# Kernel tuning notes

Measured on AMD Instinct MI355X. Metric: run time of the kernel, lower is better.

Reference implementation:

```python
import jax, jax.numpy as jnp
import numpy as np

B = 4096          # batch
D = 512           # nOut (embedding dim)
N_CLASSES = 5994  # nClasses (VoxCeleb2 speakers)


def setup_inputs() -> dict:
    key = jax.random.key(0)
    k = jax.random.split(key, 6)
    return {
        "x": jax.random.normal(k[0], (B, D), dtype=jnp.float32),
        "label": jax.random.randint(k[1], (B,), 0, N_CLASSES),
        "centers": jax.random.normal(k[2], (N_CLASSES, D), dtype=jnp.float32),
        "fc_w": jax.random.normal(k[3], (1, D), dtype=jnp.float32) / np.sqrt(D),
        "fc_b": jnp.zeros((1,), dtype=jnp.float32),
        "ch_w": jax.random.normal(k[4], (N_CLASSES, D), dtype=jnp.float32) / np.sqrt(D),
        "ch_b": jnp.zeros((N_CLASSES,), dtype=jnp.float32),
    }


def _ce(logits, labels):
    # mean cross-entropy, single stable log-softmax
    logp = jax.nn.log_softmax(logits, axis=-1)
    return -jnp.mean(jnp.take_along_axis(logp, labels[:, None], axis=-1))


def _center_add(x, label, n_classes):
    """Faithful sequential label-wise running average from the torch loop:
    first occurrence of label l: cadd[l] += x[i]; later: cadd[l] = (cadd[l]+x[i])/2.
    Sequential recurrence -> lax.scan over the batch."""
    d = x.shape[1]

    def step(carry, inp):
        cadd, seen = carry
        xi, li = inp
        first = seen[li] == 0
        row = cadd[li]
        new_row = jnp.where(first, row + xi, 0.5 * (row + xi))
        return (cadd.at[li].set(new_row), seen.at[li].set(1)), None

    init = (jnp.zeros((n_classes, d), x.dtype), jnp.zeros((n_classes,), jnp.int32))
    (cadd, seen), _ = jax.lax.scan(step, init, (x, label))
    return cadd, seen.astype(x.dtype)


def reference(x, label, centers, fc_w, fc_b, ch_w, ch_b):
    n_classes = centers.shape[0]
    cadd, label_add = _center_add(x, label, n_classes)  # label_add == labels present in batch

    alpha = jax.nn.sigmoid(centers @ fc_w.T + fc_b)[:, 0]        # [nClasses]
    center_mask = 1.0 - label_add
    gate = alpha * label_add + center_mask                        # [nClasses]
    new_center = centers * gate[:, None] + cadd * ((1.0 - alpha) * label_add)[:, None]

    center_logits = new_center @ ch_w.T + ch_b                    # [nClasses, nClasses]
    lossC = _ce(center_logits, jnp.arange(n_classes))

    output = x @ ch_w.T + ch_b                                    # [B, nClasses]
    nloss = _ce(output, label)

    prec1 = 100.0 * jnp.mean((jnp.argmax(output, axis=-1) == label).astype(jnp.float32))
    return nloss + lossC, prec1
```

## Files before the change

kernel.cpp:

```cpp
#include <hip/hip_runtime.h>

#define BB 4096
#define DD 512
#define NCC 5994
#define RBX 64
#define RBC 94
#define NSL 12
#define TPS 4
#define NBLK ((RBX + RBC) * NSL)
#define PSZ (NSL * (BB + NCC))

typedef __attribute__((ext_vector_type(8))) short bfx8;
typedef __attribute__((ext_vector_type(8))) unsigned short usx8;
typedef __attribute__((ext_vector_type(4))) float fx4;

__device__ __forceinline__ unsigned short f2bf(float f) {
    unsigned u = __builtin_bit_cast(unsigned, f);
    u += 0x7fff + ((u >> 16) & 1);
    return (unsigned short)(u >> 16);
}

__device__ __forceinline__ void gload_lds16(const void* g, void* l) {
    __builtin_amdgcn_global_load_lds(
        (const __attribute__((address_space(1))) void*)g,
        (__attribute__((address_space(3))) void*)l, 16, 0, 0);
}

__global__ void prep_kernel(const int* __restrict__ label, float* __restrict__ w,
                            float* __restrict__ label_add, const float* __restrict__ x,
                            unsigned short* __restrict__ xbuf, float* __restrict__ cadd) {
    __shared__ int lab[BB];
    int b = blockIdx.x, t = threadIdx.x;
    if (b < 16) {
        for (int j = t; j < BB; j += 256) lab[j] = label[j];
        __syncthreads();
        int i = b * 256 + t;
        int li = lab[i];
        int cnt = 0, rank = 0;
        for (int j = 0; j < BB; ++j) {
            int e = (lab[j] == li) ? 1 : 0;
            cnt += e;
            if (j < i) rank += e;
        }
        float expo = (rank == 0) ? (float)(cnt - 1) : (float)(cnt - rank);
        w[i] = exp2f(-expo);
        label_add[li] = 1.0f;
    } else if (b < 784) {
        int base = (b - 16) * 256 + t;
        float4 z = make_float4(0.f, 0.f, 0.f, 0.f);
        float4* c4 = (float4*)cadd;
#pragma unroll
        for (int k = 0; k < 4; ++k) {
            int idx = base + k * 196608;
            if (idx < (NCC * DD) / 4) c4[idx] = z;
        }
    } else {
        int i = (b - 784) * 256 + t;
        const float4* g = (const float4*)(x + (size_t)i * 8);
        float4 v0 = g[0], v1 = g[1];
        usx8 u;
        u[0] = f2bf(v0.x); u[1] = f2bf(v0.y); u[2] = f2bf(v0.z); u[3] = f2bf(v0.w);
        u[4] = f2bf(v1.x); u[5] = f2bf(v1.y); u[6] = f2bf(v1.z); u[7] = f2bf(v1.w);
        *(usx8*)(xbuf + (size_t)i * 8) = u;
    }
}

__global__ void cadd_kernel(const float* __restrict__ x, const int* __restrict__ label,
                            const float* __restrict__ w, float* __restrict__ cadd) {
    int i = blockIdx.x;
    int li = label[i];
    float wi = w[i];
    const float* xr = x + (size_t)i * DD;
    float* cr = cadd + (size_t)li * DD;
    int t = threadIdx.x;
    atomicAdd(&cr[t], wi * xr[t]);
    atomicAdd(&cr[t + 256], wi * xr[t + 256]);
}

__global__ void newcenter_kernel(const float* __restrict__ centers,
                                 const float* __restrict__ fc_w,
                                 const float* __restrict__ fc_b,
                                 const float* __restrict__ cadd,
                                 const float* __restrict__ label_add,
                                 unsigned short* __restrict__ ncb) {
    int l = blockIdx.x;
    int t = threadIdx.x;
    const float* cr = centers + (size_t)l * DD;
    float part = fmaf(cr[t], fc_w[t], cr[t + 256] * fc_w[t + 256]);
#pragma unroll
    for (int off = 32; off; off >>= 1) part += __shfl_xor(part, off);
    __shared__ float wsum[4];
    if ((t & 63) == 0) wsum[t >> 6] = part;
    __syncthreads();
    float dot = wsum[0] + wsum[1] + wsum[2] + wsum[3] + fc_b[0];
    float alpha = 1.0f / (1.0f + expf(-dot));
    float la = label_add[l];
    float gate = alpha * la + (1.0f - la);
    float beta = (1.0f - alpha) * la;
    const float* car = cadd + (size_t)l * DD;
    unsigned short* nr = ncb + (size_t)l * DD;
    nr[t]       = f2bf(fmaf(cr[t],       gate, car[t]       * beta));
    nr[t + 256] = f2bf(fmaf(cr[t + 256], gate, car[t + 256] * beta));
}

__global__ void convw_kernel(const float* __restrict__ src, unsigned short* __restrict__ dst) {
    int i = blockIdx.x * 256 + threadIdx.x;
    if (i >= NCC * DD / 8) return;
    const float4* g = (const float4*)(src + (size_t)i * 8);
    float4 v0 = g[0], v1 = g[1];
    usx8 u;
    u[0] = f2bf(v0.x); u[1] = f2bf(v0.y); u[2] = f2bf(v0.z); u[3] = f2bf(v0.w);
    u[4] = f2bf(v1.x); u[5] = f2bf(v1.y); u[6] = f2bf(v1.z); u[7] = f2bf(v1.w);
    *(usx8*)(dst + (size_t)i * 8) = u;
}

__global__ __launch_bounds__(256, 3) void mfma_ce_kernel(
    const unsigned short* __restrict__ xb, const unsigned short* __restrict__ ncb,
    const unsigned short* __restrict__ wb, const float* __restrict__ chb,
    const int* __restrict__ labelg,
    float* __restrict__ pm, float* __restrict__ ps, float* __restrict__ pt,
    float* __restrict__ pv, int* __restrict__ pi)
{
    __shared__ short lA[2][64 * 64];
    __shared__ short lB[2][128 * 64];

    int b = blockIdx.x;
    int xm, rb, slice, nrows;
    const unsigned short* src;
    if (b < RBX * NSL) { xm = 1; rb = b % RBX; slice = b / RBX; nrows = BB;  src = xb; }
    else { int c = b - RBX * NSL; xm = 0; rb = c % RBC; slice = c / RBC; nrows = NCC; src = ncb; }
    int row0  = rb * 64;
    int tile0 = slice * TPS;

    int t = threadIdx.x, lane = t & 63, wv = t >> 6;
    int wm = wv >> 1, wn = wv & 1;
    int l15 = lane & 15, l4 = lane >> 4;

    int sk8 = (lane & 7) ^ ((lane >> 3) & 7);
    int r0q = min(row0 + wv * 16 + (lane >> 3), nrows - 1);
    int r1q = min(row0 + wv * 16 + 8 + (lane >> 3), nrows - 1);
    const unsigned short* aQ0 = src + (size_t)r0q * DD + sk8 * 8;
    const unsigned short* aQ1 = src + (size_t)r1q * DD + sk8 * 8;
    int colq = wv * 32 + (lane >> 3);

    int l4x   = l4 ^ (l15 & 3);
    int ksx   = (l15 >> 2) & 1;
    int slot0 = ((0 ^ ksx) << 2) | l4x;
    int slot1 = ((1 ^ ksx) << 2) | l4x;
    int aoff0 = (wm * 32 + l15) * 128 + slot0 * 16;
    int aoff1 = (wm * 32 + l15) * 128 + slot1 * 16;
    int boff0 = (wn * 64 + l15) * 128 + slot0 * 16;
    int boff1 = (wn * 64 + l15) * 128 + slot1 * 16;

    float m_[2][4], s_[2][4], tg_[2][4], av_[2][4];
    int ai_[2][4], tc_[2][4];
#pragma unroll
    for (int mf = 0; mf < 2; ++mf)
#pragma unroll
        for (int j = 0; j < 4; ++j) {
            m_[mf][j] = -1e30f; s_[mf][j] = 0.f; tg_[mf][j] = 0.f;
            av_[mf][j] = -1e30f; ai_[mf][j] = 0x7fffffff;
            int grow = row0 + wm * 32 + mf * 16 + l4 * 4 + j;
            tc_[mf][j] = xm ? labelg[min(grow, BB - 1)] : grow;
        }

    auto stage = [&](int s, int bufIdx) {
        int tile = tile0 + (s >> 3);
        int ko = (s & 7) * 64;
        gload_lds16(aQ0 + ko, &lA[bufIdx][wv * 1024]);
        gload_lds16(aQ1 + ko, &lA[bufIdx][wv * 1024 + 512]);
        int cb = tile * 128 + colq;
#pragma unroll
        for (int q = 0; q < 4; ++q) {
            const unsigned short* bs =
                wb + (size_t)min(cb + q * 8, NCC - 1) * DD + sk8 * 8 + ko;
            gload_lds16(bs, &lB[bufIdx][wv * 2048 + q * 512]);
        }
    };

    stage(0, 0);
    __syncthreads();

    fx4 acc[2][4];
    float biasv[4];
    int buf = 0;

    for (int s = 0; s < TPS * 8; ++s) {
        int kc = s & 7;
        int tile = tile0 + (s >> 3);
        if (s + 1 < TPS * 8) stage(s + 1, buf ^ 1);
        if (kc == 0) {
#pragma unroll
            for (int mf = 0; mf < 2; ++mf)
#pragma unroll
                for (int nf = 0; nf < 4; ++nf) {
                    fx4 z = {0.f, 0.f, 0.f, 0.f};
                    acc[mf][nf] = z;
                }
#pragma unroll
            for (int nf = 0; nf < 4; ++nf) {
                int col = tile * 128 + wn * 64 + nf * 16 + l15;
                biasv[nf] = (col < NCC) ? chb[col] : 0.f;
            }
        }
        const char* Ab = (const char*)lA[buf];
        const char* Bb = (const char*)lB[buf];
        {
            bfx8 a0 = *(const bfx8*)(Ab + aoff0);
            bfx8 a1 = *(const bfx8*)(Ab + aoff0 + 2048);
            bfx8 b0 = *(const bfx8*)(Bb + boff0);
            bfx8 b1 = *(const bfx8*)(Bb + boff0 + 2048);
            bfx8 b2 = *(const bfx8*)(Bb + boff0 + 4096);
            bfx8 b3 = *(const bfx8*)(Bb + boff0 + 6144);
            acc[0][0] = __builtin_amdgcn_mfma_f32_16x16x32_bf16(a0, b0, acc[0][0], 0, 0, 0);
            acc[0][1] = __builtin_amdgcn_mfma_f32_16x16x32_bf16(a0, b1, acc[0][1], 0, 0, 0);
            acc[0][2] = __builtin_amdgcn_mfma_f32_16x16x32_bf16(a0, b2, acc[0][2], 0, 0, 0);
            acc[0][3] = __builtin_amdgcn_mfma_f32_16x16x32_bf16(a0, b3, acc[0][3], 0, 0, 0);
            acc[1][0] = __builtin_amdgcn_mfma_f32_16x16x32_bf16(a1, b0, acc[1][0], 0, 0, 0);
            acc[1][1] = __builtin_amdgcn_mfma_f32_16x16x32_bf16(a1, b1, acc[1][1], 0, 0, 0);
            acc[1][2] = __builtin_amdgcn_mfma_f32_16x16x32_bf16(a1, b2, acc[1][2], 0, 0, 0);
            acc[1][3] = __builtin_amdgcn_mfma_f32_16x16x32_bf16(a1, b3, acc[1][3], 0, 0, 0);
        }
        {
            bfx8 a0 = *(const bfx8*)(Ab + aoff1);
            bfx8 a1 = *(const bfx8*)(Ab + aoff1 + 2048);
            bfx8 b0 = *(const bfx8*)(Bb + boff1);
            bfx8 b1 = *(const bfx8*)(Bb + boff1 + 2048);
            bfx8 b2 = *(const bfx8*)(Bb + boff1 + 4096);
            bfx8 b3 = *(const bfx8*)(Bb + boff1 + 6144);
            acc[0][0] = __builtin_amdgcn_mfma_f32_16x16x32_bf16(a0, b0, acc[0][0], 0, 0, 0);
            acc[0][1] = __builtin_amdgcn_mfma_f32_16x16x32_bf16(a0, b1, acc[0][1], 0, 0, 0);
            acc[0][2] = __builtin_amdgcn_mfma_f32_16x16x32_bf16(a0, b2, acc[0][2], 0, 0, 0);
            acc[0][3] = __builtin_amdgcn_mfma_f32_16x16x32_bf16(a0, b3, acc[0][3], 0, 0, 0);
            acc[1][0] = __builtin_amdgcn_mfma_f32_16x16x32_bf16(a1, b0, acc[1][0], 0, 0, 0);
            acc[1][1] = __builtin_amdgcn_mfma_f32_16x16x32_bf16(a1, b1, acc[1][1], 0, 0, 0);
            acc[1][2] = __builtin_amdgcn_mfma_f32_16x16x32_bf16(a1, b2, acc[1][2], 0, 0, 0);
            acc[1][3] = __builtin_amdgcn_mfma_f32_16x16x32_bf16(a1, b3, acc[1][3], 0, 0, 0);
        }

        if (kc == 7) {
            int colb = tile * 128 + wn * 64 + l15;
#pragma unroll
            for (int mf = 0; mf < 2; ++mf)
#pragma unroll
                for (int j = 0; j < 4; ++j) {
                    float v0 = (colb      < NCC) ? acc[mf][0][j] + biasv[0] : -1e30f;
                    float v1 = (colb + 16 < NCC) ? acc[mf][1][j] + biasv[1] : -1e30f;
                    float v2 = (colb + 32 < NCC) ? acc[mf][2][j] + biasv[2] : -1e30f;
                    float v3 = (colb + 48 < NCC) ? acc[mf][3][j] + biasv[3] : -1e30f;
                    float cmax = fmaxf(fmaxf(v0, v1), fmaxf(v2, v3));
                    float nm = fmaxf(m_[mf][j], cmax);
                    float sacc = s_[mf][j] * __expf(m_[mf][j] - nm);
                    if (colb      < NCC) sacc += __expf(v0 - nm);
                    if (colb + 16 < NCC) sacc += __expf(v1 - nm);
                    if (colb + 32 < NCC) sacc += __expf(v2 - nm);
                    if (colb + 48 < NCC) sacc += __expf(v3 - nm);
                    s_[mf][j] = sacc;
                    m_[mf][j] = nm;
                    if (xm) {
                        if (v0 > av_[mf][j]) { av_[mf][j] = v0; ai_[mf][j] = colb; }
                        if (v1 > av_[mf][j]) { av_[mf][j] = v1; ai_[mf][j] = colb + 16; }
                        if (v2 > av_[mf][j]) { av_[mf][j] = v2; ai_[mf][j] = colb + 32; }
                        if (v3 > av_[mf][j]) { av_[mf][j] = v3; ai_[mf][j] = colb + 48; }
                    }
                    int d = tc_[mf][j] - colb;
                    if (d == 0)  tg_[mf][j] = v0;
                    if (d == 16) tg_[mf][j] = v1;
                    if (d == 32) tg_[mf][j] = v2;
                    if (d == 48) tg_[mf][j] = v3;
                }
        }
        __syncthreads();
        buf ^= 1;
    }

#pragma unroll
    for (int off = 1; off < 16; off <<= 1) {
#pragma unroll
        for (int mf = 0; mf < 2; ++mf)
#pragma unroll
            for (int j = 0; j < 4; ++j) {
                float om = __shfl_xor(m_[mf][j], off);
                float os = __shfl_xor(s_[mf][j], off);
                float ot = __shfl_xor(tg_[mf][j], off);
                float ov = __shfl_xor(av_[mf][j], off);
                int   oi = __shfl_xor(ai_[mf][j], off);
                float nm = fmaxf(m_[mf][j], om);
                s_[mf][j] = s_[mf][j] * __expf(m_[mf][j] - nm) + os * __expf(om - nm);
                m_[mf][j] = nm;
                tg_[mf][j] += ot;
                if (ov > av_[mf][j] || (ov == av_[mf][j] && oi < ai_[mf][j])) {
                    av_[mf][j] = ov; ai_[mf][j] = oi;
                }
            }
    }

    float* red = (float*)lB;
    int* redi = (int*)(red + 512);
    if (l15 == 0) {
#pragma unroll
        for (int mf = 0; mf < 2; ++mf)
#pragma unroll
            for (int j = 0; j < 4; ++j) {
                int rowloc = wm * 32 + mf * 16 + l4 * 4 + j;
                int idx = wn * 64 + rowloc;
                red[idx]       = m_[mf][j];
                red[128 + idx] = s_[mf][j];
                red[256 + idx] = tg_[mf][j];
                red[384 + idx] = av_[mf][j];
                redi[idx]      = ai_[mf][j];
            }
    }
    __syncthreads();
    if (t < 64) {
        int grow = row0 + t;
        if (grow < nrows) {
            float M = red[t], S = red[128 + t], T = red[256 + t];
            float V = red[384 + t]; int I = redi[t];
            float m2 = red[64 + t], s2 = red[192 + t];
            float nm = fmaxf(M, m2);
            S = S * __expf(M - nm) + s2 * __expf(m2 - nm); M = nm;
            T += red[320 + t];
            float v2 = red[448 + t]; int i2 = redi[64 + t];
            if (v2 > V || (v2 == V && i2 < I)) { V = v2; I = i2; }
            int pidx = xm ? (grow * NSL + slice) : (BB * NSL + grow * NSL + slice);
            pm[pidx] = M; ps[pidx] = S; pt[pidx] = T; pv[pidx] = V; pi[pidx] = I;
        }
    }
}

__global__ void merge_kernel(const float* __restrict__ pm, const float* __restrict__ ps,
                             const float* __restrict__ pt, const float* __restrict__ pv,
                             const int* __restrict__ pi, const int* __restrict__ label,
                             float* __restrict__ sums) {
    int tid = blockIdx.x * 256 + threadIdx.x;
    float ce = 0.f, corr = 0.f;
    int isx = (tid < BB) ? 1 : 0;
    int base = -1;
    if (tid < BB) base = tid * NSL;
    else if (tid < BB + NCC) base = BB * NSL + (tid - BB) * NSL;
    if (base >= 0) {
        float M = -1e30f, S = 0.f, T = 0.f, V = -1e30f; int I = 0x7fffffff;
#pragma unroll
        for (int s2 = 0; s2 < NSL; ++s2) {
            float m = pm[base + s2], s = ps[base + s2];
            float nm = fmaxf(M, m);
            S = S * __expf(M - nm) + s * __expf(m - nm); M = nm;
            T += pt[base + s2];
            float v = pv[base + s2]; int i2 = pi[base + s2];
            if (v > V || (v == V && i2 < I)) { V = v; I = i2; }
        }
        ce = -(T - M - logf(S));
        if (isx) corr = (I == label[tid]) ? 1.f : 0.f;
    }
#pragma unroll
    for (int off = 32; off; off >>= 1) {
        ce += __shfl_xor(ce, off);
        corr += __shfl_xor(corr, off);
    }
    if ((threadIdx.x & 63) == 0) {
        atomicAdd(&sums[isx ? 0 : 2], ce);
        if (isx) atomicAdd(&sums[1], corr);
    }
}

__global__ void finalize_kernel(const float* __restrict__ sums, float* __restrict__ out) {
    out[0] = sums[0] / (float)BB + sums[2] / (float)NCC;
    out[1] = 100.0f * sums[1] / (float)BB;
}

extern "C" void kernel_launch(void* const* d_in, const int* in_sizes, int n_in,
                              void* d_out, int out_size, void* d_ws, size_t ws_size,
                              hipStream_t stream) {
    const float* x       = (const float*)d_in[0];
    const int*   label   = (const int*)d_in[1];
    const float* centers = (const float*)d_in[2];
    const float* fc_w    = (const float*)d_in[3];
    const float* fc_b    = (const float*)d_in[4];
    const float* ch_w    = (const float*)d_in[5];
    const float* ch_b    = (const float*)d_in[6];
    float* out = (float*)d_out;

    float* ws = (float*)d_ws;
    float* w         = ws;
    float* label_add = ws + 4096;
    float* sums      = ws + 10090;
    float* cadd      = ws + 14192;
    float* pm        = ws + 14192;
    float* ps        = pm + PSZ;
    float* pt        = ps + PSZ;
    float* pv        = pt + PSZ;
    int*   pi        = (int*)(pv + PSZ);
    unsigned short* wbuf  = (unsigned short*)(ws + 619592);
    unsigned short* xbuf  = (unsigned short*)(ws + 3084144);
    unsigned short* ncbuf = (unsigned short*)(ws + 4132720);

    hipMemsetAsync(label_add, 0, 6000 * sizeof(float), stream);

    prep_kernel<<<1808, 256, 0, stream>>>(label, w, label_add, x, xbuf, cadd);
    cadd_kernel<<<BB, 256, 0, stream>>>(x, label, w, cadd);
    newcenter_kernel<<<NCC, 256, 0, stream>>>(centers, fc_w, fc_b, cadd, label_add, ncbuf);
    convw_kernel<<<(NCC * DD / 8 + 255) / 256, 256, 0, stream>>>(ch_w, wbuf);

    mfma_ce_kernel<<<NBLK, 256, 0, stream>>>(xbuf, ncbuf, wbuf, ch_b, label,
                                             pm, ps, pt, pv, pi);

    merge_kernel<<<(BB + NCC + 255) / 256, 256, 0, stream>>>(pm, ps, pt, pv, pi, label, sums);
    finalize_kernel<<<1, 1, 0, stream>>>(sums, out);
}
```

Baseline: 315.0 us.

## Restructure GEMM main loop with explicit waitcnt barriers, hoisted bias, merged argmax

Splits the K loop into an unrolled tile loop with an inner k-chunk loop, replaces __syncthreads with a partial vmcnt wait plus raw s_barrier so the next stage's global-to-LDS loads stay in flight, and raises wave priority around the MFMA block. Bias values for all four tiles are preloaded into registers up front. The separate argmax value tracker is dropped and the argmax index now rides on the running softmax max, which removes registers, shuffles and LDS traffic. It also issues a wasted wraparound stage on the last step, and correctness depends on the vmcnt count matching the six loads per stage.

New measurement: 366.5 us. +16.3%, slower.

```diff
diff --git a/kernel.cpp b/kernel.cpp
--- a/kernel.cpp
+++ b/kernel.cpp
@@ -152,14 +152,23 @@
     int boff0 = (wn * 64 + l15) * 128 + slot0 * 16;
     int boff1 = (wn * 64 + l15) * 128 + slot1 * 16;
 
-    float m_[2][4], s_[2][4], tg_[2][4], av_[2][4];
+    float bva[4][4];
+#pragma unroll
+    for (int tt = 0; tt < 4; ++tt)
+#pragma unroll
+        for (int nf = 0; nf < 4; ++nf) {
+            int col = (tile0 + tt) * 128 + wn * 64 + nf * 16 + l15;
+            bva[tt][nf] = (col < NCC) ? chb[col] : 0.f;
+        }
+
+    float m_[2][4], s_[2][4], tg_[2][4];
     int ai_[2][4], tc_[2][4];
 #pragma unroll
     for (int mf = 0; mf < 2; ++mf)
 #pragma unroll
         for (int j = 0; j < 4; ++j) {
             m_[mf][j] = -1e30f; s_[mf][j] = 0.f; tg_[mf][j] = 0.f;
-            av_[mf][j] = -1e30f; ai_[mf][j] = 0x7fffffff;
+            ai_[mf][j] = 0x7fffffff;
             int grow = row0 + wm * 32 + mf * 16 + l4 * 4 + j;
             tc_[mf][j] = xm ? labelg[min(grow, BB - 1)] : grow;
         }
@@ -179,39 +188,44 @@
     };
 
     stage(0, 0);
-    __syncthreads();
 
     fx4 acc[2][4];
-    float biasv[4];
     int buf = 0;
 
-    for (int s = 0; s < TPS * 8; ++s) {
-        int kc = s & 7;
-        int tile = tile0 + (s >> 3);
-        if (s + 1 < TPS * 8) stage(s + 1, buf ^ 1);
-        if (kc == 0) {
-#pragma unroll
-            for (int mf = 0; mf < 2; ++mf)
-#pragma unroll
-                for (int nf = 0; nf < 4; ++nf) {
-                    fx4 z = {0.f, 0.f, 0.f, 0.f};
-                    acc[mf][nf] = z;
-                }
+#pragma unroll
+    for (int tt = 0; tt < 4; ++tt) {
+#pragma unroll
+        for (int mf = 0; mf < 2; ++mf)
 #pragma unroll
             for (int nf = 0; nf < 4; ++nf) {
-                int col = tile * 128 + wn * 64 + nf * 16 + l15;
-                biasv[nf] = (col < NCC) ? chb[col] : 0.f;
+                fx4 z = {0.f, 0.f, 0.f, 0.f};
+                acc[mf][nf] = z;
             }
-        }
-        const char* Ab = (const char*)lA[buf];
-        const char* Bb = (const char*)lB[buf];
-        {
+
+        for (int s2 = 0; s2 < 8; ++s2) {
+            int step = tt * 8 + s2;
+            int nxt = (step + 1 < 32) ? step + 1 : 0;
+            stage(nxt, buf ^ 1);
+            asm volatile("s_waitcnt vmcnt(6)" ::: "memory");
+            __builtin_amdgcn_s_barrier();
+            __builtin_amdgcn_sched_barrier(0);
+
+            const char* Ab = (const char*)lA[buf];
+            const char* Bb = (const char*)lB[buf];
             bfx8 a0 = *(const bfx8*)(Ab + aoff0);
             bfx8 a1 = *(const bfx8*)(Ab + aoff0 + 2048);
             bfx8 b0 = *(const bfx8*)(Bb + boff0);
             bfx8 b1 = *(const bfx8*)(Bb + boff0 + 2048);
             bfx8 b2 = *(const bfx8*)(Bb + boff0 + 4096);
             bfx8 b3 = *(const bfx8*)(Bb + boff0 + 6144);
+            bfx8 a2 = *(const bfx8*)(Ab + aoff1);
+            bfx8 a3 = *(const bfx8*)(Ab + aoff1 + 2048);
+            bfx8 b4 = *(const bfx8*)(Bb + boff1);
+            bfx8 b5 = *(const bfx8*)(Bb + boff1 + 2048);
+            bfx8 b6 = *(const bfx8*)(Bb + boff1 + 4096);
+            bfx8 b7 = *(const bfx8*)(Bb + boff1 + 6144);
+
+            __builtin_amdgcn_s_setprio(1);
             acc[0][0] = __builtin_amdgcn_mfma_f32_16x16x32_bf16(a0, b0, acc[0][0], 0, 0, 0);
             acc[0][1] = __builtin_amdgcn_mfma_f32_16x16x32_bf16(a0, b1, acc[0][1], 0, 0, 0);
             acc[0][2] = __builtin_amdgcn_mfma_f32_16x16x32_bf16(a0, b2, acc[0][2], 0, 0, 0);
@@ -220,49 +234,43 @@
             acc[1][1] = __builtin_amdgcn_mfma_f32_16x16x32_bf16(a1, b1, acc[1][1], 0, 0, 0);
             acc[1][2] = __builtin_amdgcn_mfma_f32_16x16x32_bf16(a1, b2, acc[1][2], 0, 0, 0);
             acc[1][3] = __builtin_amdgcn_mfma_f32_16x16x32_bf16(a1, b3, acc[1][3], 0, 0, 0);
-        }
+            acc[0][0] = __builtin_amdgcn_mfma_f32_16x16x32_bf16(a2, b4, acc[0][0], 0, 0, 0);
+            acc[0][1] = __builtin_amdgcn_mfma_f32_16x16x32_bf16(a2, b5, acc[0][1], 0, 0, 0);
+            acc[0][2] = __builtin_amdgcn_mfma_f32_16x16x32_bf16(a2, b6, acc[0][2], 0, 0, 0);
+            acc[0][3] = __builtin_amdgcn_mfma_f32_16x16x32_bf16(a2, b7, acc[0][3], 0, 0, 0);
+            acc[1][0] = __builtin_amdgcn_mfma_f32_16x16x32_bf16(a3, b4, acc[1][0], 0, 0, 0);
+            acc[1][1] = __builtin_amdgcn_mfma_f32_16x16x32_bf16(a3, b5, acc[1][1], 0, 0, 0);
+            acc[1][2] = __builtin_amdgcn_mfma_f32_16x16x32_bf16(a3, b6, acc[1][2], 0, 0, 0);
+            acc[1][3] = __builtin_amdgcn_mfma_f32_16x16x32_bf16(a3, b7, acc[1][3], 0, 0, 0);
+            __builtin_amdgcn_s_setprio(0);
+
+            __builtin_amdgcn_s_barrier();
+            buf ^= 1;
+        }
+
         {
-            bfx8 a0 = *(const bfx8*)(Ab + aoff1);
-            bfx8 a1 = *(const bfx8*)(Ab + aoff1 + 2048);
-            bfx8 b0 = *(const bfx8*)(Bb + boff1);
-            bfx8 b1 = *(const bfx8*)(Bb + boff1 + 2048);
-            bfx8 b2 = *(const bfx8*)(Bb + boff1 + 4096);
-            bfx8 b3 = *(const bfx8*)(Bb + boff1 + 6144);
-            acc[0][0] = __builtin_amdgcn_mfma_f32_16x16x32_bf16(a0, b0, acc[0][0], 0, 0, 0);
-            acc[0][1] = __builtin_amdgcn_mfma_f32_16x16x32_bf16(a0, b1, acc[0][1], 0, 0, 0);
-            acc[0][2] = __builtin_amdgcn_mfma_f32_16x16x32_bf16(a0, b2, acc[0][2], 0, 0, 0);
-            acc[0][3] = __builtin_amdgcn_mfma_f32_16x16x32_bf16(a0, b3, acc[0][3], 0, 0, 0);
-            acc[1][0] = __builtin_amdgcn_mfma_f32_16x16x32_bf16(a1, b0, acc[1][0], 0, 0, 0);
-            acc[1][1] = __builtin_amdgcn_mfma_f32_16x16x32_bf16(a1, b1, acc[1][1], 0, 0, 0);
-            acc[1][2] = __builtin_amdgcn_mfma_f32_16x16x32_bf16(a1, b2, acc[1][2], 0, 0, 0);
-            acc[1][3] = __builtin_amdgcn_mfma_f32_16x16x32_bf16(a1, b3, acc[1][3], 0, 0, 0);
-        }
-
-        if (kc == 7) {
-            int colb = tile * 128 + wn * 64 + l15;
+            int colb = (tile0 + tt) * 128 + wn * 64 + l15;
 #pragma unroll
             for (int mf = 0; mf < 2; ++mf)
 #pragma unroll
                 for (int j = 0; j < 4; ++j) {
-                    float v0 = (colb      < NCC) ? acc[mf][0][j] + biasv[0] : -1e30f;
-                    float v1 = (colb + 16 < NCC) ? acc[mf][1][j] + biasv[1] : -1e30f;
-                    float v2 = (colb + 32 < NCC) ? acc[mf][2][j] + biasv[2] : -1e30f;
-                    float v3 = (colb + 48 < NCC) ? acc[mf][3][j] + biasv[3] : -1e30f;
-                    float cmax = fmaxf(fmaxf(v0, v1), fmaxf(v2, v3));
-                    float nm = fmaxf(m_[mf][j], cmax);
+                    float v0 = (colb      < NCC) ? acc[mf][0][j] + bva[tt][0] : -1e30f;
+                    float v1 = (colb + 16 < NCC) ? acc[mf][1][j] + bva[tt][1] : -1e30f;
+                    float v2 = (colb + 32 < NCC) ? acc[mf][2][j] + bva[tt][2] : -1e30f;
+                    float v3 = (colb + 48 < NCC) ? acc[mf][3][j] + bva[tt][3] : -1e30f;
+                    float tv = v0; int tcol = colb;
+                    if (v1 > tv) { tv = v1; tcol = colb + 16; }
+                    if (v2 > tv) { tv = v2; tcol = colb + 32; }
+                    if (v3 > tv) { tv = v3; tcol = colb + 48; }
+                    float nm = fmaxf(m_[mf][j], tv);
                     float sacc = s_[mf][j] * __expf(m_[mf][j] - nm);
                     if (colb      < NCC) sacc += __expf(v0 - nm);
                     if (colb + 16 < NCC) sacc += __expf(v1 - nm);
                     if (colb + 32 < NCC) sacc += __expf(v2 - nm);
                     if (colb + 48 < NCC) sacc += __expf(v3 - nm);
                     s_[mf][j] = sacc;
+                    if (xm && tv > m_[mf][j]) ai_[mf][j] = tcol;
                     m_[mf][j] = nm;
-                    if (xm) {
-                        if (v0 > av_[mf][j]) { av_[mf][j] = v0; ai_[mf][j] = colb; }
-                        if (v1 > av_[mf][j]) { av_[mf][j] = v1; ai_[mf][j] = colb + 16; }
-                        if (v2 > av_[mf][j]) { av_[mf][j] = v2; ai_[mf][j] = colb + 32; }
-                        if (v3 > av_[mf][j]) { av_[mf][j] = v3; ai_[mf][j] = colb + 48; }
-                    }
                     int d = tc_[mf][j] - colb;
                     if (d == 0)  tg_[mf][j] = v0;
                     if (d == 16) tg_[mf][j] = v1;
@@ -270,9 +278,9 @@
                     if (d == 48) tg_[mf][j] = v3;
                 }
         }
-        __syncthreads();
-        buf ^= 1;
-    }
+    }
+
+    __syncthreads();
 
 #pragma unroll
     for (int off = 1; off < 16; off <<= 1) {
@@ -283,20 +291,18 @@
                 float om = __shfl_xor(m_[mf][j], off);
                 float os = __shfl_xor(s_[mf][j], off);
                 float ot = __shfl_xor(tg_[mf][j], off);
-                float ov = __shfl_xor(av_[mf][j], off);
                 int   oi = __shfl_xor(ai_[mf][j], off);
                 float nm = fmaxf(m_[mf][j], om);
                 s_[mf][j] = s_[mf][j] * __expf(m_[mf][j] - nm) + os * __expf(om - nm);
+                if (om > m_[mf][j] || (om == m_[mf][j] && oi < ai_[mf][j]))
+                    ai_[mf][j] = oi;
                 m_[mf][j] = nm;
                 tg_[mf][j] += ot;
-                if (ov > av_[mf][j] || (ov == av_[mf][j] && oi < ai_[mf][j])) {
-                    av_[mf][j] = ov; ai_[mf][j] = oi;
-                }
             }
     }
 
     float* red = (float*)lB;
-    int* redi = (int*)(red + 512);
+    int* redi = (int*)(red + 384);
     if (l15 == 0) {
 #pragma unroll
         for (int mf = 0; mf < 2; ++mf)
@@ -307,7 +313,6 @@
                 red[idx]       = m_[mf][j];
                 red[128 + idx] = s_[mf][j];
                 red[256 + idx] = tg_[mf][j];
-                red[384 + idx] = av_[mf][j];
                 redi[idx]      = ai_[mf][j];
             }
     }
@@ -316,15 +321,16 @@
         int grow = row0 + t;
         if (grow < nrows) {
             float M = red[t], S = red[128 + t], T = red[256 + t];
-            float V = red[384 + t]; int I = redi[t];
+            int I = redi[t];
             float m2 = red[64 + t], s2 = red[192 + t];
+            int i2 = redi[64 + t];
             float nm = fmaxf(M, m2);
-            S = S * __expf(M - nm) + s2 * __expf(m2 - nm); M = nm;
+            S = S * __expf(M - nm) + s2 * __expf(m2 - nm);
+            if (m2 > M || (m2 == M && i2 < I)) I = i2;
+            M = nm;
             T += red[320 + t];
-            float v2 = red[448 + t]; int i2 = redi[64 + t];
-            if (v2 > V || (v2 == V && i2 < I)) { V = v2; I = i2; }
             int pidx = xm ? (grow * NSL + slice) : (BB * NSL + grow * NSL + slice);
-            pm[pidx] = M; ps[pidx] = S; pt[pidx] = T; pv[pidx] = V; pi[pidx] = I;
+            pm[pidx] = M; ps[pidx] = S; pt[pidx] = T; pv[pidx] = M; pi[pidx] = I;
         }
     }
 }
```
